# Performance work log

Measured on AMD Instinct MI355X. Metric: run time of the kernel, lower is better.

The kernel has to match this reference:

```python
import jax, jax.numpy as jnp
import numpy as np

N_NODES = 25000
N_EDGES = 320000
IN_FEAT = 64
OUT_FEAT = 64
NUM_HEADS = 5
NUM_RELS = 20
NUM_BASES = 10


def setup_inputs() -> dict:
    key = jax.random.key(0)
    ks = jax.random.split(key, 8)
    feat = jax.random.normal(ks[0], (N_NODES, IN_FEAT), dtype=jnp.float32)
    src = jax.random.randint(ks[1], (N_EDGES,), 0, N_NODES, dtype=jnp.int64 if jax.config.jax_enable_x64 else jnp.int32)
    dst = jax.random.randint(ks[2], (N_EDGES,), 0, N_NODES, dtype=src.dtype)
    edge_type = jax.random.randint(ks[3], (N_EDGES,), 0, NUM_RELS, dtype=src.dtype)
    fc_w = jax.random.normal(ks[4], (IN_FEAT, OUT_FEAT), dtype=jnp.float32) * (2.0 / np.sqrt(IN_FEAT + OUT_FEAT))
    self_fc_w = jax.random.normal(ks[5], (IN_FEAT, NUM_HEADS * OUT_FEAT), dtype=jnp.float32) * (2.0 / np.sqrt(IN_FEAT + NUM_HEADS * OUT_FEAT))
    attention_weight = jax.random.normal(ks[6], (NUM_BASES, 2 * OUT_FEAT, NUM_HEADS), dtype=jnp.float32) * (2.0 / np.sqrt(2 * OUT_FEAT + NUM_HEADS))
    w_comp = jax.random.normal(ks[7], (NUM_RELS, NUM_BASES), dtype=jnp.float32) * (2.0 / np.sqrt(NUM_RELS + NUM_BASES))
    return {"feat": feat, "src": src, "dst": dst, "edge_type": edge_type,
            "fc_w": fc_w, "self_fc_w": self_fc_w,
            "attention_weight": attention_weight, "w_comp": w_comp}


def reference(feat, src, dst, edge_type, fc_w, self_fc_w, attention_weight, w_comp):
    # node projections
    z = feat @ fc_w                      # [N, F]
    self_z = feat @ self_fc_w            # [N, H*F]
    # basis-composed per-relation attention matrices: [R, 2F, H]
    attn_fcs = jnp.einsum('rb,bfh->rfh', w_comp, attention_weight)
    # per-edge attention: cat(src_z, dst_z) bmm gathered relation matrix
    z2 = jnp.concatenate([z[src], z[dst]], axis=1)          # [E, 2F]
    w_e = attn_fcs[edge_type]                                # [E, 2F, H] irregular gather
    att = jax.nn.leaky_relu(jnp.einsum('ef,efh->eh', z2, w_e), negative_slope=0.01)  # [E, H]
    # message = outer(att, src_z) flattened, segment-summed over dst
    msg = (att[:, :, None] * z[src][:, None, :]).reshape(att.shape[0], -1)  # [E, H*F]
    h = jax.ops.segment_sum(msg, dst, num_segments=feat.shape[0])            # [N, H*F]
    h = h + self_z  # self interaction; activation is None
    return h
```

## Files before the change

### kernel.cpp

```cpp
#include <hip/hip_runtime.h>
#include <hip/hip_bf16.h>

#define N_NODES 25000
#define N_EDGES 320000
#define F 64
#define H 5
#define R 20
#define B 10
#define HF 320
#define MPAD 25008
#define CAP 64

typedef __attribute__((ext_vector_type(8))) short short8;
typedef __attribute__((ext_vector_type(4))) short short4v;
typedef __attribute__((ext_vector_type(4))) float float4v;

__device__ __forceinline__ float ldf(const void* p, int f32, int i) {
    if (f32) return ((const float*)p)[i];
    else     return __bfloat162float(((const __hip_bfloat16*)p)[i]);
}
__device__ __forceinline__ int ldi(const void* p, int i64, int i) {
    if (i64) return ((const int*)p)[2 * i];
    else     return ((const int*)p)[i];
}
__device__ __forceinline__ float b2f(unsigned short u) {
    union { unsigned u32; float f; } v; v.u32 = ((unsigned)u) << 16; return v.f;
}
__device__ __forceinline__ short f2bs(float x) {
    __hip_bfloat16 v = __float2bfloat16(x); return *(short*)&v;
}

__device__ __forceinline__ int probe_f32(const void* feat_raw) {
    unsigned w = ((const unsigned*)feat_raw)[threadIdx.x & 63];
    unsigned e = (w >> 7) & 0xFF;
    unsigned long long m = __ballot(e >= 110 && e <= 140);
    return __popcll(m) < 32;
}
__device__ __forceinline__ int probe_i64(const void* src_raw) {
    unsigned v = ((const unsigned*)src_raw)[2 * (threadIdx.x & 63) + 1];
    unsigned long long m = __ballot(v == 0);
    return __popcll(m) > 32;
}

__global__ void k0_setup(const void* __restrict__ feat,
                         const void* __restrict__ fcw, const void* __restrict__ sfw,
                         const void* __restrict__ aw, const void* __restrict__ wc,
                         __hip_bfloat16* __restrict__ Wpack,
                         __hip_bfloat16* __restrict__ W2pack,
                         int* __restrict__ cnt) {
    const int f32 = probe_f32(feat);
    const int b = blockIdx.x, tid = threadIdx.x;
    if (b < 176) {
        const int idx = b * 256 + tid;
        if (idx < 24576) {
            int j = idx & 7, lane = (idx >> 3) & 63, fq = idx >> 9;
            int q = fq & 1, t = fq >> 1;
            int k = (q ? 32 : 0) + ((lane >> 4) << 3) + j;
            int c = t * 16 + (lane & 15);
            float v = (c < HF) ? ldf(sfw, f32, k * HF + c) : ldf(fcw, f32, k * F + (c - HF));
            Wpack[idx] = __float2bfloat16(v);
        } else if (idx < 24576 + 20480) {
            int id2 = idx - 24576;
            int j = id2 & 7, lane = (id2 >> 3) & 63, fq = id2 >> 9;
            int q = fq & 1, t = fq >> 1;
            int k = (q ? 32 : 0) + ((lane >> 4) << 3) + j;
            int c = t * 16 + (lane & 15);
            int r = c >> 4, part = (c >> 3) & 1, h = c & 7;
            float acc = 0.f;
            if (h < H) {
#pragma unroll
                for (int bb = 0; bb < B; ++bb)
                    acc += ldf(wc, f32, r * B + bb) *
                           ldf(aw, f32, bb * (2 * F * H) + (part * F + k) * H + h);
            }
            W2pack[id2] = __float2bfloat16(acc);
        }
    } else {
        const int i = (b - 176) * 256 + tid;
        if (i < N_NODES) cnt[i] = 0;
    }
}

__global__ __launch_bounds__(256) void k2_gemm(const void* __restrict__ feat,
                                               const void* __restrict__ srcp,
                                               const void* __restrict__ dstp,
                                               const void* __restrict__ etp,
                                               const __hip_bfloat16* __restrict__ Wpack,
                                               const __hip_bfloat16* __restrict__ W2pack,
                                               __hip_bfloat16* __restrict__ selfz,
                                               __hip_bfloat16* __restrict__ zc,
                                               __hip_bfloat16* __restrict__ a_src,
                                               __hip_bfloat16* __restrict__ a_dst,
                                               int* __restrict__ cnt,
                                               unsigned* __restrict__ perm) {
    __shared__ short zl[16][66];
    const int tid = threadIdx.x;

    if (blockIdx.x >= 1563) {
        const int i64 = probe_i64(srcp);
        const int e = (blockIdx.x - 1563) * 256 + tid;
        if (e < N_EDGES) {
            int d = ldi(dstp, i64, e);
            int s = ldi(srcp, i64, e);
            int r = ldi(etp, i64, e);
            int pos = atomicAdd(&cnt[d], 1);
            if (pos < CAP) perm[d * CAP + pos] = ((unsigned)r << 16) | (unsigned)s;
        }
        return;
    }

    const int f32 = probe_f32(feat);
    const int wave = tid >> 6, lane = tid & 63;
    const int quad = lane >> 4, col = lane & 15;
    const int r0 = blockIdx.x * 16;
    int am = r0 + col;
    if (am >= N_NODES) am = N_NODES - 1;
    const int row = r0 + col;

    short8 a0, a1;
    if (f32) {
        const float* Af = (const float*)feat;
        float4v f0 = *(const float4v*)(Af + am * F + quad * 8);
        float4v f1 = *(const float4v*)(Af + am * F + quad * 8 + 4);
        float4v g0 = *(const float4v*)(Af + am * F + 32 + quad * 8);
        float4v g1 = *(const float4v*)(Af + am * F + 32 + quad * 8 + 4);
#pragma unroll
        for (int j = 0; j < 4; ++j) {
            a0[j] = f2bs(f0[j]); a0[j + 4] = f2bs(f1[j]);
            a1[j] = f2bs(g0[j]); a1[j + 4] = f2bs(g1[j]);
        }
    } else {
        const __hip_bfloat16* A = (const __hip_bfloat16*)feat;
        a0 = *(const short8*)(A + am * F + quad * 8);
        a1 = *(const short8*)(A + am * F + 32 + quad * 8);
    }

    const short8* Wp = (const short8*)Wpack;

    {
        const int t = 20 + wave;
        short8 b0 = Wp[(t * 2 + 0) * 64 + lane];
        short8 b1 = Wp[(t * 2 + 1) * 64 + lane];
        float4v acc = {0.f, 0.f, 0.f, 0.f};
        acc = __builtin_amdgcn_mfma_f32_16x16x32_bf16(b0, a0, acc, 0, 0, 0);
        acc = __builtin_amdgcn_mfma_f32_16x16x32_bf16(b1, a1, acc, 0, 0, 0);
        short4v pv;
#pragma unroll
        for (int j = 0; j < 4; ++j) pv[j] = f2bs(acc[j]);
        const int cb = wave * 16 + quad * 4;
        *(short4v*)(zc + row * F + cb) = pv;
        *(short4v*)&zl[col][cb] = pv;
    }
    __syncthreads();

    short8 c0 = *(const short8*)&zl[col][quad * 8];
    short8 c1 = *(const short8*)&zl[col][32 + quad * 8];

#pragma unroll
    for (int tt = 0; tt < 5; ++tt) {
        const int t = wave * 5 + tt;
        short8 b0 = Wp[(t * 2 + 0) * 64 + lane];
        short8 b1 = Wp[(t * 2 + 1) * 64 + lane];
        float4v acc = {0.f, 0.f, 0.f, 0.f};
        acc = __builtin_amdgcn_mfma_f32_16x16x32_bf16(b0, a0, acc, 0, 0, 0);
        acc = __builtin_amdgcn_mfma_f32_16x16x32_bf16(b1, a1, acc, 0, 0, 0);
        short4v pv;
#pragma unroll
        for (int j = 0; j < 4; ++j) pv[j] = f2bs(acc[j]);
        *(short4v*)(selfz + row * HF + t * 16 + quad * 4) = pv;
    }

    const short8* W2p = (const short8*)W2pack;
    __hip_bfloat16* dsta = (quad & 2) ? a_dst : a_src;
    const int hoff = (quad & 1) * 4;
#pragma unroll
    for (int tt = 0; tt < 5; ++tt) {
        const int t = wave * 5 + tt;
        short8 b0 = W2p[(t * 2 + 0) * 64 + lane];
        short8 b1 = W2p[(t * 2 + 1) * 64 + lane];
        float4v acc = {0.f, 0.f, 0.f, 0.f};
        acc = __builtin_amdgcn_mfma_f32_16x16x32_bf16(b0, c0, acc, 0, 0, 0);
        acc = __builtin_amdgcn_mfma_f32_16x16x32_bf16(b1, c1, acc, 0, 0, 0);
        short4v pv;
#pragma unroll
        for (int j = 0; j < 4; ++j) pv[j] = f2bs(acc[j]);
        *(short4v*)(dsta + row * 160 + t * 8 + hoff) = pv;
    }
}

__global__ __launch_bounds__(256) void k4_agg(const void* __restrict__ feat_raw,
                                              const __hip_bfloat16* __restrict__ selfz,
                                              const unsigned short* __restrict__ zc,
                                              const __hip_bfloat16* __restrict__ a_src,
                                              const __hip_bfloat16* __restrict__ a_dst,
                                              const int* __restrict__ cnt,
                                              const unsigned* __restrict__ perm,
                                              void* __restrict__ out) {
    __shared__ short sdv[4][160];
    const int f32 = probe_f32(feat_raw);
    const int tid = threadIdx.x;
    const int wid = tid >> 6, lane = tid & 63;
    const int d = blockIdx.x * 4 + wid;

    if (lane < 20)
        *(short8*)&sdv[wid][lane * 8] = *(const short8*)((const short*)a_dst + d * 160 + lane * 8);

    int mypk = (int)perm[d * CAP + lane];
    int n = cnt[d];
    if (n > CAP) n = CAP;
    __syncthreads();

    const short* as = (const short*)a_src;

    float acc[H] = {0.f, 0.f, 0.f, 0.f, 0.f};
    int e = 0;
    for (; e + 4 <= n; e += 4) {
        int s_[4], r_[4];
#pragma unroll
        for (int u = 0; u < 4; ++u) {
            unsigned pk = (unsigned)__shfl(mypk, e + u);
            s_[u] = (int)(pk & 0xFFFFu); r_[u] = (int)(pk >> 16);
        }
        short8 sv[4];
        float zs[4];
#pragma unroll
        for (int u = 0; u < 4; ++u) sv[u] = *(const short8*)(as + s_[u] * 160 + r_[u] * 8);
#pragma unroll
        for (int u = 0; u < 4; ++u) zs[u] = b2f(zc[s_[u] * F + lane]);
        short8 dv[4];
#pragma unroll
        for (int u = 0; u < 4; ++u) dv[u] = *(const short8*)&sdv[wid][r_[u] * 8];
#pragma unroll
        for (int u = 0; u < 4; ++u) {
#pragma unroll
            for (int h = 0; h < H; ++h) {
                float t = b2f((unsigned short)sv[u][h]) + b2f((unsigned short)dv[u][h]);
                acc[h] += fmaxf(t, 0.01f * t) * zs[u];
            }
        }
    }
    for (; e < n; ++e) {
        unsigned pk = (unsigned)__shfl(mypk, e);
        const int s = (int)(pk & 0xFFFFu), r = (int)(pk >> 16);
        short8 sv = *(const short8*)(as + s * 160 + r * 8);
        const float zs = b2f(zc[s * F + lane]);
        short8 dv = *(const short8*)&sdv[wid][r * 8];
#pragma unroll
        for (int h = 0; h < H; ++h) {
            float t = b2f((unsigned short)sv[h]) + b2f((unsigned short)dv[h]);
            acc[h] += fmaxf(t, 0.01f * t) * zs;
        }
    }

    const int ob = d * HF + lane;
    if (f32) {
        float* o = (float*)out;
#pragma unroll
        for (int h = 0; h < H; ++h)
            o[ob + h * F] = acc[h] + __bfloat162float(selfz[ob + h * F]);
    } else {
        __hip_bfloat16* o = (__hip_bfloat16*)out;
#pragma unroll
        for (int h = 0; h < H; ++h)
            o[ob + h * F] = __float2bfloat16(acc[h] + __bfloat162float(selfz[ob + h * F]));
    }
}

extern "C" void kernel_launch(void* const* d_in, const int* in_sizes, int n_in,
                              void* d_out, int out_size, void* d_ws, size_t ws_size,
                              hipStream_t stream) {
    const void* feat = d_in[0];
    const void* src  = d_in[1];
    const void* dst  = d_in[2];
    const void* et   = d_in[3];
    const void* fcw  = d_in[4];
    const void* sfw  = d_in[5];
    const void* aw   = d_in[6];
    const void* wc   = d_in[7];

    char* w = (char*)d_ws;
    __hip_bfloat16* selfz  = (__hip_bfloat16*)w;  w += (size_t)MPAD * HF * 2;
    __hip_bfloat16* zc     = (__hip_bfloat16*)w;  w += (size_t)MPAD * F * 2;
    __hip_bfloat16* a_src  = (__hip_bfloat16*)w;  w += (size_t)MPAD * 160 * 2;
    __hip_bfloat16* a_dst  = (__hip_bfloat16*)w;  w += (size_t)MPAD * 160 * 2;
    __hip_bfloat16* Wpack  = (__hip_bfloat16*)w;  w += 24576 * 2;
    __hip_bfloat16* W2pack = (__hip_bfloat16*)w;  w += 20480 * 2;
    unsigned* perm = (unsigned*)w;                w += (size_t)N_NODES * CAP * 4;
    int* cnt       = (int*)w;

    k0_setup<<<176 + (N_NODES + 255) / 256, 256, 0, stream>>>(feat, fcw, sfw, aw, wc,
                                                              Wpack, W2pack, cnt);
    k2_gemm<<<1563 + (N_EDGES + 255) / 256, 256, 0, stream>>>(feat, src, dst, et,
                                                              Wpack, W2pack, selfz, zc,
                                                              a_src, a_dst, cnt, perm);
    k4_agg<<<N_NODES / 4, 256, 0, stream>>>(feat, selfz, (const unsigned short*)zc,
                                            a_src, a_dst, cnt, perm, d_out);
}
```

Before: 140.6 us.

## Tile GEMM blocks over 64 rows and precompute per-edge attention in LDS

```diff
diff --git a/kernel.cpp b/kernel.cpp
--- a/kernel.cpp
+++ b/kernel.cpp
@@ -8,12 +8,14 @@
 #define R 20
 #define B 10
 #define HF 320
-#define MPAD 25008
+#define GEMMB 391
+#define MPAD 25024
 #define CAP 64
 
 typedef __attribute__((ext_vector_type(8))) short short8;
 typedef __attribute__((ext_vector_type(4))) short short4v;
 typedef __attribute__((ext_vector_type(4))) float float4v;
+typedef __attribute__((ext_vector_type(2))) float float2v;
 
 __device__ __forceinline__ float ldf(const void* p, int f32, int i) {
     if (f32) return ((const float*)p)[i];
@@ -93,12 +95,12 @@
                                                __hip_bfloat16* __restrict__ a_dst,
                                                int* __restrict__ cnt,
                                                unsigned* __restrict__ perm) {
-    __shared__ short zl[16][66];
+    __shared__ short zl[64][66];
     const int tid = threadIdx.x;
 
-    if (blockIdx.x >= 1563) {
+    if (blockIdx.x >= GEMMB) {
         const int i64 = probe_i64(srcp);
-        const int e = (blockIdx.x - 1563) * 256 + tid;
+        const int e = (blockIdx.x - GEMMB) * 256 + tid;
         if (e < N_EDGES) {
             int d = ldi(dstp, i64, e);
             int s = ldi(srcp, i64, e);
@@ -112,27 +114,29 @@
     const int f32 = probe_f32(feat);
     const int wave = tid >> 6, lane = tid & 63;
     const int quad = lane >> 4, col = lane & 15;
-    const int r0 = blockIdx.x * 16;
-    int am = r0 + col;
-    if (am >= N_NODES) am = N_NODES - 1;
-    const int row = r0 + col;
-
-    short8 a0, a1;
-    if (f32) {
-        const float* Af = (const float*)feat;
-        float4v f0 = *(const float4v*)(Af + am * F + quad * 8);
-        float4v f1 = *(const float4v*)(Af + am * F + quad * 8 + 4);
-        float4v g0 = *(const float4v*)(Af + am * F + 32 + quad * 8);
-        float4v g1 = *(const float4v*)(Af + am * F + 32 + quad * 8 + 4);
-#pragma unroll
-        for (int j = 0; j < 4; ++j) {
-            a0[j] = f2bs(f0[j]); a0[j + 4] = f2bs(f1[j]);
-            a1[j] = f2bs(g0[j]); a1[j + 4] = f2bs(g1[j]);
-        }
-    } else {
-        const __hip_bfloat16* A = (const __hip_bfloat16*)feat;
-        a0 = *(const short8*)(A + am * F + quad * 8);
-        a1 = *(const short8*)(A + am * F + 32 + quad * 8);
+    const int r0 = blockIdx.x * 64;
+
+    short8 a0g[4], a1g[4];
+#pragma unroll
+    for (int g = 0; g < 4; ++g) {
+        int am = r0 + g * 16 + col;
+        if (am >= N_NODES) am = N_NODES - 1;
+        if (f32) {
+            const float* Af = (const float*)feat;
+            float4v f0 = *(const float4v*)(Af + am * F + quad * 8);
+            float4v f1 = *(const float4v*)(Af + am * F + quad * 8 + 4);
+            float4v g0 = *(const float4v*)(Af + am * F + 32 + quad * 8);
+            float4v g1 = *(const float4v*)(Af + am * F + 32 + quad * 8 + 4);
+#pragma unroll
+            for (int j = 0; j < 4; ++j) {
+                a0g[g][j] = f2bs(f0[j]); a0g[g][j + 4] = f2bs(f1[j]);
+                a1g[g][j] = f2bs(g0[j]); a1g[g][j + 4] = f2bs(g1[j]);
+            }
+        } else {
+            const __hip_bfloat16* A = (const __hip_bfloat16*)feat;
+            a0g[g] = *(const short8*)(A + am * F + quad * 8);
+            a1g[g] = *(const short8*)(A + am * F + 32 + quad * 8);
+        }
     }
 
     const short8* Wp = (const short8*)Wpack;
@@ -141,33 +145,45 @@
         const int t = 20 + wave;
         short8 b0 = Wp[(t * 2 + 0) * 64 + lane];
         short8 b1 = Wp[(t * 2 + 1) * 64 + lane];
-        float4v acc = {0.f, 0.f, 0.f, 0.f};
-        acc = __builtin_amdgcn_mfma_f32_16x16x32_bf16(b0, a0, acc, 0, 0, 0);
-        acc = __builtin_amdgcn_mfma_f32_16x16x32_bf16(b1, a1, acc, 0, 0, 0);
-        short4v pv;
-#pragma unroll
-        for (int j = 0; j < 4; ++j) pv[j] = f2bs(acc[j]);
         const int cb = wave * 16 + quad * 4;
-        *(short4v*)(zc + row * F + cb) = pv;
-        *(short4v*)&zl[col][cb] = pv;
+#pragma unroll
+        for (int g = 0; g < 4; ++g) {
+            float4v acc = {0.f, 0.f, 0.f, 0.f};
+            acc = __builtin_amdgcn_mfma_f32_16x16x32_bf16(b0, a0g[g], acc, 0, 0, 0);
+            acc = __builtin_amdgcn_mfma_f32_16x16x32_bf16(b1, a1g[g], acc, 0, 0, 0);
+            short4v pv;
+#pragma unroll
+            for (int j = 0; j < 4; ++j) pv[j] = f2bs(acc[j]);
+            const int row = r0 + g * 16 + col;
+            *(short4v*)(zc + row * F + cb) = pv;
+            *(short4v*)&zl[g * 16 + col][cb] = pv;
+        }
     }
     __syncthreads();
 
-    short8 c0 = *(const short8*)&zl[col][quad * 8];
-    short8 c1 = *(const short8*)&zl[col][32 + quad * 8];
+    short8 c0g[4], c1g[4];
+#pragma unroll
+    for (int g = 0; g < 4; ++g) {
+        c0g[g] = *(const short8*)&zl[g * 16 + col][quad * 8];
+        c1g[g] = *(const short8*)&zl[g * 16 + col][32 + quad * 8];
+    }
 
 #pragma unroll
     for (int tt = 0; tt < 5; ++tt) {
         const int t = wave * 5 + tt;
         short8 b0 = Wp[(t * 2 + 0) * 64 + lane];
         short8 b1 = Wp[(t * 2 + 1) * 64 + lane];
-        float4v acc = {0.f, 0.f, 0.f, 0.f};
-        acc = __builtin_amdgcn_mfma_f32_16x16x32_bf16(b0, a0, acc, 0, 0, 0);
-        acc = __builtin_amdgcn_mfma_f32_16x16x32_bf16(b1, a1, acc, 0, 0, 0);
-        short4v pv;
-#pragma unroll
-        for (int j = 0; j < 4; ++j) pv[j] = f2bs(acc[j]);
-        *(short4v*)(selfz + row * HF + t * 16 + quad * 4) = pv;
+#pragma unroll
+        for (int g = 0; g < 4; ++g) {
+            float4v acc = {0.f, 0.f, 0.f, 0.f};
+            acc = __builtin_amdgcn_mfma_f32_16x16x32_bf16(b0, a0g[g], acc, 0, 0, 0);
+            acc = __builtin_amdgcn_mfma_f32_16x16x32_bf16(b1, a1g[g], acc, 0, 0, 0);
+            short4v pv;
+#pragma unroll
+            for (int j = 0; j < 4; ++j) pv[j] = f2bs(acc[j]);
+            const int row = r0 + g * 16 + col;
+            *(short4v*)(selfz + row * HF + t * 16 + quad * 4) = pv;
+        }
     }
 
     const short8* W2p = (const short8*)W2pack;
@@ -178,13 +194,17 @@
         const int t = wave * 5 + tt;
         short8 b0 = W2p[(t * 2 + 0) * 64 + lane];
         short8 b1 = W2p[(t * 2 + 1) * 64 + lane];
-        float4v acc = {0.f, 0.f, 0.f, 0.f};
-        acc = __builtin_amdgcn_mfma_f32_16x16x32_bf16(b0, c0, acc, 0, 0, 0);
-        acc = __builtin_amdgcn_mfma_f32_16x16x32_bf16(b1, c1, acc, 0, 0, 0);
-        short4v pv;
-#pragma unroll
-        for (int j = 0; j < 4; ++j) pv[j] = f2bs(acc[j]);
-        *(short4v*)(dsta + row * 160 + t * 8 + hoff) = pv;
+#pragma unroll
+        for (int g = 0; g < 4; ++g) {
+            float4v acc = {0.f, 0.f, 0.f, 0.f};
+            acc = __builtin_amdgcn_mfma_f32_16x16x32_bf16(b0, c0g[g], acc, 0, 0, 0);
+            acc = __builtin_amdgcn_mfma_f32_16x16x32_bf16(b1, c1g[g], acc, 0, 0, 0);
+            short4v pv;
+#pragma unroll
+            for (int j = 0; j < 4; ++j) pv[j] = f2bs(acc[j]);
+            const int row = r0 + g * 16 + col;
+            *(short4v*)(dsta + row * 160 + t * 8 + hoff) = pv;
+        }
     }
 }
 
@@ -197,6 +217,7 @@
                                               const unsigned* __restrict__ perm,
                                               void* __restrict__ out) {
     __shared__ short sdv[4][160];
+    __shared__ float satt[4][CAP][8];
     const int f32 = probe_f32(feat_raw);
     const int tid = threadIdx.x;
     const int wid = tid >> 6, lane = tid & 63;
@@ -204,52 +225,58 @@
 
     if (lane < 20)
         *(short8*)&sdv[wid][lane * 8] = *(const short8*)((const short*)a_dst + d * 160 + lane * 8);
-
-    int mypk = (int)perm[d * CAP + lane];
+    const unsigned pk = perm[d * CAP + lane];
+    const int s_l = (int)(pk & 0xFFFFu), r_l = (int)(pk >> 16);
     int n = cnt[d];
     if (n > CAP) n = CAP;
     __syncthreads();
 
     const short* as = (const short*)a_src;
 
+    if (lane < n) {
+        short8 sv = *(const short8*)(as + s_l * 160 + r_l * 8);
+        short8 dv = *(const short8*)&sdv[wid][r_l * 8];
+        float av[H];
+#pragma unroll
+        for (int h = 0; h < H; ++h) {
+            float t = b2f((unsigned short)sv[h]) + b2f((unsigned short)dv[h]);
+            av[h] = fmaxf(t, 0.01f * t);
+        }
+        float4v w0 = {av[0], av[1], av[2], av[3]};
+        *(float4v*)&satt[wid][lane][0] = w0;
+        float2v w1 = {av[4], __int_as_float(s_l)};
+        *(float2v*)&satt[wid][lane][4] = w1;
+    }
+    __syncthreads();
+
     float acc[H] = {0.f, 0.f, 0.f, 0.f, 0.f};
     int e = 0;
     for (; e + 4 <= n; e += 4) {
-        int s_[4], r_[4];
+        float4v A[4]; float2v Bv[4];
 #pragma unroll
         for (int u = 0; u < 4; ++u) {
-            unsigned pk = (unsigned)__shfl(mypk, e + u);
-            s_[u] = (int)(pk & 0xFFFFu); r_[u] = (int)(pk >> 16);
-        }
-        short8 sv[4];
+            A[u] = *(const float4v*)&satt[wid][e + u][0];
+            Bv[u] = *(const float2v*)&satt[wid][e + u][4];
+        }
         float zs[4];
 #pragma unroll
-        for (int u = 0; u < 4; ++u) sv[u] = *(const short8*)(as + s_[u] * 160 + r_[u] * 8);
-#pragma unroll
-        for (int u = 0; u < 4; ++u) zs[u] = b2f(zc[s_[u] * F + lane]);
-        short8 dv[4];
-#pragma unroll
-        for (int u = 0; u < 4; ++u) dv[u] = *(const short8*)&sdv[wid][r_[u] * 8];
+        for (int u = 0; u < 4; ++u)
+            zs[u] = b2f(zc[__float_as_int(Bv[u][1]) * F + lane]);
 #pragma unroll
         for (int u = 0; u < 4; ++u) {
-#pragma unroll
-            for (int h = 0; h < H; ++h) {
-                float t = b2f((unsigned short)sv[u][h]) + b2f((unsigned short)dv[u][h]);
-                acc[h] += fmaxf(t, 0.01f * t) * zs[u];
-            }
+            acc[0] += A[u][0] * zs[u];
+            acc[1] += A[u][1] * zs[u];
+            acc[2] += A[u][2] * zs[u];
+            acc[3] += A[u][3] * zs[u];
+            acc[4] += Bv[u][0] * zs[u];
         }
     }
     for (; e < n; ++e) {
-        unsigned pk = (unsigned)__shfl(mypk, e);
-        const int s = (int)(pk & 0xFFFFu), r = (int)(pk >> 16);
-        short8 sv = *(const short8*)(as + s * 160 + r * 8);
-        const float zs = b2f(zc[s * F + lane]);
-        short8 dv = *(const short8*)&sdv[wid][r * 8];
-#pragma unroll
-        for (int h = 0; h < H; ++h) {
-            float t = b2f((unsigned short)sv[h]) + b2f((unsigned short)dv[h]);
-            acc[h] += fmaxf(t, 0.01f * t) * zs;
-        }
+        float4v A = *(const float4v*)&satt[wid][e][0];
+        float2v Bv = *(const float2v*)&satt[wid][e][4];
+        float zs = b2f(zc[__float_as_int(Bv[1]) * F + lane]);
+        acc[0] += A[0] * zs; acc[1] += A[1] * zs; acc[2] += A[2] * zs;
+        acc[3] += A[3] * zs; acc[4] += Bv[0] * zs;
     }
 
     const int ob = d * HF + lane;
@@ -290,9 +317,9 @@
 
     k0_setup<<<176 + (N_NODES + 255) / 256, 256, 0, stream>>>(feat, fcw, sfw, aw, wc,
                                                               Wpack, W2pack, cnt);
-    k2_gemm<<<1563 + (N_EDGES + 255) / 256, 256, 0, stream>>>(feat, src, dst, et,
-                                                              Wpack, W2pack, selfz, zc,
-                                                              a_src, a_dst, cnt, perm);
+    k2_gemm<<<GEMMB + (N_EDGES + 255) / 256, 256, 0, stream>>>(feat, src, dst, et,
+                                                               Wpack, W2pack, selfz, zc,
+                                                               a_src, a_dst, cnt, perm);
     k4_agg<<<N_NODES / 4, 256, 0, stream>>>(feat, selfz, (const unsigned short*)zc,
                                             a_src, a_dst, cnt, perm, d_out);
 }
```

Measured after the change: 134.5 us (median of 2 runs). 4.3% less time.

## Fuse three kernels into one persistent kernel with grid barriers

Applied to the files above, without the earlier changes.

```diff
diff --git a/kernel.cpp b/kernel.cpp
--- a/kernel.cpp
+++ b/kernel.cpp
@@ -8,12 +8,16 @@
 #define R 20
 #define B 10
 #define HF 320
-#define MPAD 25008
+#define MPAD 25024
 #define CAP 64
+#define GRID 1024
+#define GEMMV 1563
+#define SCATV 1250
 
 typedef __attribute__((ext_vector_type(8))) short short8;
 typedef __attribute__((ext_vector_type(4))) short short4v;
 typedef __attribute__((ext_vector_type(4))) float float4v;
+typedef __attribute__((ext_vector_type(2))) float float2v;
 
 __device__ __forceinline__ float ldf(const void* p, int f32, int i) {
     if (f32) return ((const float*)p)[i];
@@ -42,227 +46,237 @@
     return __popcll(m) > 32;
 }
 
-__global__ void k0_setup(const void* __restrict__ feat,
-                         const void* __restrict__ fcw, const void* __restrict__ sfw,
-                         const void* __restrict__ aw, const void* __restrict__ wc,
-                         __hip_bfloat16* __restrict__ Wpack,
-                         __hip_bfloat16* __restrict__ W2pack,
-                         int* __restrict__ cnt) {
+__device__ __forceinline__ void gridbar(int* bar) {
+    __syncthreads();
+    if (threadIdx.x == 0) {
+        __threadfence();
+        atomicAdd(bar, 1);
+        while (__hip_atomic_load(bar, __ATOMIC_RELAXED, __HIP_MEMORY_SCOPE_AGENT) < GRID)
+            __builtin_amdgcn_s_sleep(2);
+        __threadfence();
+    }
+    __syncthreads();
+}
+
+__global__ __launch_bounds__(256, 4) void mega(
+    const void* __restrict__ feat, const void* __restrict__ srcp,
+    const void* __restrict__ dstp, const void* __restrict__ etp,
+    const void* __restrict__ fcw, const void* __restrict__ sfw,
+    const void* __restrict__ aw, const void* __restrict__ wc,
+    __hip_bfloat16* __restrict__ Wpack, __hip_bfloat16* __restrict__ W2pack,
+    __hip_bfloat16* __restrict__ selfz, __hip_bfloat16* __restrict__ zc,
+    __hip_bfloat16* __restrict__ a_src, __hip_bfloat16* __restrict__ a_dst,
+    int* __restrict__ cnt, unsigned* __restrict__ perm,
+    int* __restrict__ bar, void* __restrict__ out)
+{
+    __shared__ union SM {
+        short zl[16][66];
+        struct P2 { short sdv[4][160]; float satt[4][CAP][8]; } p2;
+    } sm;
+
+    const int tid = threadIdx.x;
     const int f32 = probe_f32(feat);
-    const int b = blockIdx.x, tid = threadIdx.x;
-    if (b < 176) {
-        const int idx = b * 256 + tid;
-        if (idx < 24576) {
-            int j = idx & 7, lane = (idx >> 3) & 63, fq = idx >> 9;
-            int q = fq & 1, t = fq >> 1;
-            int k = (q ? 32 : 0) + ((lane >> 4) << 3) + j;
-            int c = t * 16 + (lane & 15);
-            float v = (c < HF) ? ldf(sfw, f32, k * HF + c) : ldf(fcw, f32, k * F + (c - HF));
-            Wpack[idx] = __float2bfloat16(v);
-        } else if (idx < 24576 + 20480) {
-            int id2 = idx - 24576;
-            int j = id2 & 7, lane = (id2 >> 3) & 63, fq = id2 >> 9;
-            int q = fq & 1, t = fq >> 1;
-            int k = (q ? 32 : 0) + ((lane >> 4) << 3) + j;
-            int c = t * 16 + (lane & 15);
-            int r = c >> 4, part = (c >> 3) & 1, h = c & 7;
-            float acc = 0.f;
-            if (h < H) {
-#pragma unroll
-                for (int bb = 0; bb < B; ++bb)
-                    acc += ldf(wc, f32, r * B + bb) *
-                           ldf(aw, f32, bb * (2 * F * H) + (part * F + k) * H + h);
-            }
-            W2pack[id2] = __float2bfloat16(acc);
-        }
-    } else {
-        const int i = (b - 176) * 256 + tid;
-        if (i < N_NODES) cnt[i] = 0;
-    }
-}
-
-__global__ __launch_bounds__(256) void k2_gemm(const void* __restrict__ feat,
-                                               const void* __restrict__ srcp,
-                                               const void* __restrict__ dstp,
-                                               const void* __restrict__ etp,
-                                               const __hip_bfloat16* __restrict__ Wpack,
-                                               const __hip_bfloat16* __restrict__ W2pack,
-                                               __hip_bfloat16* __restrict__ selfz,
-                                               __hip_bfloat16* __restrict__ zc,
-                                               __hip_bfloat16* __restrict__ a_src,
-                                               __hip_bfloat16* __restrict__ a_dst,
-                                               int* __restrict__ cnt,
-                                               unsigned* __restrict__ perm) {
-    __shared__ short zl[16][66];
-    const int tid = threadIdx.x;
-
-    if (blockIdx.x >= 1563) {
-        const int i64 = probe_i64(srcp);
-        const int e = (blockIdx.x - 1563) * 256 + tid;
-        if (e < N_EDGES) {
-            int d = ldi(dstp, i64, e);
-            int s = ldi(srcp, i64, e);
-            int r = ldi(etp, i64, e);
-            int pos = atomicAdd(&cnt[d], 1);
-            if (pos < CAP) perm[d * CAP + pos] = ((unsigned)r << 16) | (unsigned)s;
-        }
-        return;
-    }
-
-    const int f32 = probe_f32(feat);
+    const int i64 = probe_i64(srcp);
     const int wave = tid >> 6, lane = tid & 63;
     const int quad = lane >> 4, col = lane & 15;
-    const int r0 = blockIdx.x * 16;
-    int am = r0 + col;
-    if (am >= N_NODES) am = N_NODES - 1;
-    const int row = r0 + col;
-
-    short8 a0, a1;
-    if (f32) {
-        const float* Af = (const float*)feat;
-        float4v f0 = *(const float4v*)(Af + am * F + quad * 8);
-        float4v f1 = *(const float4v*)(Af + am * F + quad * 8 + 4);
-        float4v g0 = *(const float4v*)(Af + am * F + 32 + quad * 8);
-        float4v g1 = *(const float4v*)(Af + am * F + 32 + quad * 8 + 4);
-#pragma unroll
-        for (int j = 0; j < 4; ++j) {
-            a0[j] = f2bs(f0[j]); a0[j + 4] = f2bs(f1[j]);
-            a1[j] = f2bs(g0[j]); a1[j + 4] = f2bs(g1[j]);
-        }
-    } else {
-        const __hip_bfloat16* A = (const __hip_bfloat16*)feat;
-        a0 = *(const short8*)(A + am * F + quad * 8);
-        a1 = *(const short8*)(A + am * F + 32 + quad * 8);
+
+    {
+        const int vb = blockIdx.x;
+        if (vb < 176) {
+            const int idx = vb * 256 + tid;
+            if (idx < 24576) {
+                int j = idx & 7, ln = (idx >> 3) & 63, fq = idx >> 9;
+                int q = fq & 1, t = fq >> 1;
+                int k = (q ? 32 : 0) + ((ln >> 4) << 3) + j;
+                int c = t * 16 + (ln & 15);
+                float v = (c < HF) ? ldf(sfw, f32, k * HF + c) : ldf(fcw, f32, k * F + (c - HF));
+                Wpack[idx] = __float2bfloat16(v);
+            } else if (idx < 24576 + 20480) {
+                int id2 = idx - 24576;
+                int j = id2 & 7, ln = (id2 >> 3) & 63, fq = id2 >> 9;
+                int q = fq & 1, t = fq >> 1;
+                int k = (q ? 32 : 0) + ((ln >> 4) << 3) + j;
+                int c = t * 16 + (ln & 15);
+                int r = c >> 4, part = (c >> 3) & 1, h = c & 7;
+                float acc = 0.f;
+                if (h < H) {
+#pragma unroll
+                    for (int bb = 0; bb < B; ++bb)
+                        acc += ldf(wc, f32, r * B + bb) *
+                               ldf(aw, f32, bb * (2 * F * H) + (part * F + k) * H + h);
+                }
+                W2pack[id2] = __float2bfloat16(acc);
+            }
+        } else if (vb < 274) {
+            const int i = (vb - 176) * 256 + tid;
+            if (i < N_NODES) cnt[i] = 0;
+        }
     }
-
-    const short8* Wp = (const short8*)Wpack;
-
-    {
-        const int t = 20 + wave;
-        short8 b0 = Wp[(t * 2 + 0) * 64 + lane];
-        short8 b1 = Wp[(t * 2 + 1) * 64 + lane];
-        float4v acc = {0.f, 0.f, 0.f, 0.f};
-        acc = __builtin_amdgcn_mfma_f32_16x16x32_bf16(b0, a0, acc, 0, 0, 0);
-        acc = __builtin_amdgcn_mfma_f32_16x16x32_bf16(b1, a1, acc, 0, 0, 0);
-        short4v pv;
-#pragma unroll
-        for (int j = 0; j < 4; ++j) pv[j] = f2bs(acc[j]);
-        const int cb = wave * 16 + quad * 4;
-        *(short4v*)(zc + row * F + cb) = pv;
-        *(short4v*)&zl[col][cb] = pv;
+    gridbar(&bar[0]);
+
+    for (int vb = blockIdx.x; vb < GEMMV + SCATV; vb += GRID) {
+        if (vb >= GEMMV) {
+            const int e = (vb - GEMMV) * 256 + tid;
+            if (e < N_EDGES) {
+                int d = ldi(dstp, i64, e);
+                int s = ldi(srcp, i64, e);
+                int r = ldi(etp, i64, e);
+                int pos = atomicAdd(&cnt[d], 1);
+                if (pos < CAP) perm[d * CAP + pos] = ((unsigned)r << 16) | (unsigned)s;
+            }
+            continue;
+        }
+
+        int am = vb * 16 + col;
+        if (am >= N_NODES) am = N_NODES - 1;
+        const int row = vb * 16 + col;
+
+        short8 a0, a1;
+        if (f32) {
+            const float* Af = (const float*)feat;
+            float4v f0 = *(const float4v*)(Af + am * F + quad * 8);
+            float4v f1 = *(const float4v*)(Af + am * F + quad * 8 + 4);
+            float4v g0 = *(const float4v*)(Af + am * F + 32 + quad * 8);
+            float4v g1 = *(const float4v*)(Af + am * F + 32 + quad * 8 + 4);
+#pragma unroll
+            for (int j = 0; j < 4; ++j) {
+                a0[j] = f2bs(f0[j]); a0[j + 4] = f2bs(f1[j]);
+                a1[j] = f2bs(g0[j]); a1[j + 4] = f2bs(g1[j]);
+            }
+        } else {
+            const __hip_bfloat16* A = (const __hip_bfloat16*)feat;
+            a0 = *(const short8*)(A + am * F + quad * 8);
+            a1 = *(const short8*)(A + am * F + 32 + quad * 8);
+        }
+
+        const short8* Wp = (const short8*)Wpack;
+
+        {
+            const int t = 20 + wave;
+            short8 b0 = Wp[(t * 2 + 0) * 64 + lane];
+            short8 b1 = Wp[(t * 2 + 1) * 64 + lane];
+            float4v acc = {0.f, 0.f, 0.f, 0.f};
+            acc = __builtin_amdgcn_mfma_f32_16x16x32_bf16(b0, a0, acc, 0, 0, 0);
+            acc = __builtin_amdgcn_mfma_f32_16x16x32_bf16(b1, a1, acc, 0, 0, 0);
+            short4v pv;
+#pragma unroll
+            for (int j = 0; j < 4; ++j) pv[j] = f2bs(acc[j]);
+            const int cb = wave * 16 + quad * 4;
+            *(short4v*)(zc + row * F + cb) = pv;
+            *(short4v*)&sm.zl[col][cb] = pv;
+        }
+        __syncthreads();
+
+        short8 c0 = *(const short8*)&sm.zl[col][quad * 8];
+        short8 c1 = *(const short8*)&sm.zl[col][32 + quad * 8];
+
+#pragma unroll
+        for (int tt = 0; tt < 5; ++tt) {
+            const int t = wave * 5 + tt;
+            short8 b0 = Wp[(t * 2 + 0) * 64 + lane];
+            short8 b1 = Wp[(t * 2 + 1) * 64 + lane];
+            float4v acc = {0.f, 0.f, 0.f, 0.f};
+            acc = __builtin_amdgcn_mfma_f32_16x16x32_bf16(b0, a0, acc, 0, 0, 0);
+            acc = __builtin_amdgcn_mfma_f32_16x16x32_bf16(b1, a1, acc, 0, 0, 0);
+            short4v pv;
+#pragma unroll
+            for (int j = 0; j < 4; ++j) pv[j] = f2bs(acc[j]);
+            *(short4v*)(selfz + row * HF + t * 16 + quad * 4) = pv;
+        }
+
+        const short8* W2p = (const short8*)W2pack;
+        __hip_bfloat16* dsta = (quad & 2) ? a_dst : a_src;
+        const int hoff = (quad & 1) * 4;
+#pragma unroll
+        for (int tt = 0; tt < 5; ++tt) {
+            const int t = wave * 5 + tt;
+            short8 b0 = W2p[(t * 2 + 0) * 64 + lane];
+            short8 b1 = W2p[(t * 2 + 1) * 64 + lane];
+            float4v acc = {0.f, 0.f, 0.f, 0.f};
+            acc = __builtin_amdgcn_mfma_f32_16x16x32_bf16(b0, c0, acc, 0, 0, 0);
+            acc = __builtin_amdgcn_mfma_f32_16x16x32_bf16(b1, c1, acc, 0, 0, 0);
+            short4v pv;
+#pragma unroll
+            for (int j = 0; j < 4; ++j) pv[j] = f2bs(acc[j]);
+            *(short4v*)(dsta + row * 160 + t * 8 + hoff) = pv;
+        }
+        __syncthreads();
     }
-    __syncthreads();
-
-    short8 c0 = *(const short8*)&zl[col][quad * 8];
-    short8 c1 = *(const short8*)&zl[col][32 + quad * 8];
-
-#pragma unroll
-    for (int tt = 0; tt < 5; ++tt) {
-        const int t = wave * 5 + tt;
-        short8 b0 = Wp[(t * 2 + 0) * 64 + lane];
-        short8 b1 = Wp[(t * 2 + 1) * 64 + lane];
-        float4v acc = {0.f, 0.f, 0.f, 0.f};
-        acc = __builtin_amdgcn_mfma_f32_16x16x32_bf16(b0, a0, acc, 0, 0, 0);
-        acc = __builtin_amdgcn_mfma_f32_16x16x32_bf16(b1, a1, acc, 0, 0, 0);
-        short4v pv;
-#pragma unroll
-        for (int j = 0; j < 4; ++j) pv[j] = f2bs(acc[j]);
-        *(short4v*)(selfz + row * HF + t * 16 + quad * 4) = pv;
-    }
-
-    const short8* W2p = (const short8*)W2pack;
-    __hip_bfloat16* dsta = (quad & 2) ? a_dst : a_src;
-    const int hoff = (quad & 1) * 4;
-#pragma unroll
-    for (int tt = 0; tt < 5; ++tt) {
-        const int t = wave * 5 + tt;
-        short8 b0 = W2p[(t * 2 + 0) * 64 + lane];
-        short8 b1 = W2p[(t * 2 + 1) * 64 + lane];
-        float4v acc = {0.f, 0.f, 0.f, 0.f};
-        acc = __builtin_amdgcn_mfma_f32_16x16x32_bf16(b0, c0, acc, 0, 0, 0);
-        acc = __builtin_amdgcn_mfma_f32_16x16x32_bf16(b1, c1, acc, 0, 0, 0);
-        short4v pv;
-#pragma unroll
-        for (int j = 0; j < 4; ++j) pv[j] = f2bs(acc[j]);
-        *(short4v*)(dsta + row * 160 + t * 8 + hoff) = pv;
-    }
-}
-
-__global__ __launch_bounds__(256) void k4_agg(const void* __restrict__ feat_raw,
-                                              const __hip_bfloat16* __restrict__ selfz,
-                                              const unsigned short* __restrict__ zc,
-                                              const __hip_bfloat16* __restrict__ a_src,
-                                              const __hip_bfloat16* __restrict__ a_dst,
-                                              const int* __restrict__ cnt,
-                                              const unsigned* __restrict__ perm,
-                                              void* __restrict__ out) {
-    __shared__ short sdv[4][160];
-    const int f32 = probe_f32(feat_raw);
-    const int tid = threadIdx.x;
-    const int wid = tid >> 6, lane = tid & 63;
-    const int d = blockIdx.x * 4 + wid;
-
-    if (lane < 20)
-        *(short8*)&sdv[wid][lane * 8] = *(const short8*)((const short*)a_dst + d * 160 + lane * 8);
-
-    int mypk = (int)perm[d * CAP + lane];
-    int n = cnt[d];
-    if (n > CAP) n = CAP;
-    __syncthreads();
-
-    const short* as = (const short*)a_src;
-
-    float acc[H] = {0.f, 0.f, 0.f, 0.f, 0.f};
-    int e = 0;
-    for (; e + 4 <= n; e += 4) {
-        int s_[4], r_[4];
-#pragma unroll
-        for (int u = 0; u < 4; ++u) {
-            unsigned pk = (unsigned)__shfl(mypk, e + u);
-            s_[u] = (int)(pk & 0xFFFFu); r_[u] = (int)(pk >> 16);
-        }
-        short8 sv[4];
-        float zs[4];
-#pragma unroll
-        for (int u = 0; u < 4; ++u) sv[u] = *(const short8*)(as + s_[u] * 160 + r_[u] * 8);
-#pragma unroll
-        for (int u = 0; u < 4; ++u) zs[u] = b2f(zc[s_[u] * F + lane]);
-        short8 dv[4];
-#pragma unroll
-        for (int u = 0; u < 4; ++u) dv[u] = *(const short8*)&sdv[wid][r_[u] * 8];
-#pragma unroll
-        for (int u = 0; u < 4; ++u) {
+    gridbar(&bar[1]);
+
+    for (int vb = blockIdx.x; vb < N_NODES / 4; vb += GRID) {
+        const int d = vb * 4 + wave;
+
+        if (lane < 20)
+            *(short8*)&sm.p2.sdv[wave][lane * 8] =
+                *(const short8*)((const short*)a_dst + d * 160 + lane * 8);
+        const unsigned pk = perm[d * CAP + lane];
+        const int s_l = (int)(pk & 0xFFFFu), r_l = (int)(pk >> 16);
+        int n = cnt[d];
+        if (n > CAP) n = CAP;
+        __syncthreads();
+
+        const short* as = (const short*)a_src;
+
+        if (lane < n) {
+            short8 sv = *(const short8*)(as + s_l * 160 + r_l * 8);
+            short8 dv = *(const short8*)&sm.p2.sdv[wave][r_l * 8];
+            float av[H];
 #pragma unroll
             for (int h = 0; h < H; ++h) {
-                float t = b2f((unsigned short)sv[u][h]) + b2f((unsigned short)dv[u][h]);
-                acc[h] += fmaxf(t, 0.01f * t) * zs[u];
-            }
-        }
-    }
-    for (; e < n; ++e) {
-        unsigned pk = (unsigned)__shfl(mypk, e);
-        const int s = (int)(pk & 0xFFFFu), r = (int)(pk >> 16);
-        short8 sv = *(const short8*)(as + s * 160 + r * 8);
-        const float zs = b2f(zc[s * F + lane]);
-        short8 dv = *(const short8*)&sdv[wid][r * 8];
-#pragma unroll
-        for (int h = 0; h < H; ++h) {
-            float t = b2f((unsigned short)sv[h]) + b2f((unsigned short)dv[h]);
-            acc[h] += fmaxf(t, 0.01f * t) * zs;
-        }
-    }
-
-    const int ob = d * HF + lane;
-    if (f32) {
-        float* o = (float*)out;
-#pragma unroll
-        for (int h = 0; h < H; ++h)
-            o[ob + h * F] = acc[h] + __bfloat162float(selfz[ob + h * F]);
-    } else {
-        __hip_bfloat16* o = (__hip_bfloat16*)out;
-#pragma unroll
-        for (int h = 0; h < H; ++h)
-            o[ob + h * F] = __float2bfloat16(acc[h] + __bfloat162float(selfz[ob + h * F]));
+                float t = b2f((unsigned short)sv[h]) + b2f((unsigned short)dv[h]);
+                av[h] = fmaxf(t, 0.01f * t);
+            }
+            float4v w0 = {av[0], av[1], av[2], av[3]};
+            *(float4v*)&sm.p2.satt[wave][lane][0] = w0;
+            float2v w1 = {av[4], __int_as_float(s_l)};
+            *(float2v*)&sm.p2.satt[wave][lane][4] = w1;
+        }
+        __syncthreads();
+
+        float acc[H] = {0.f, 0.f, 0.f, 0.f, 0.f};
+        int e = 0;
+        for (; e + 4 <= n; e += 4) {
+            float4v A[4]; float2v Bv[4];
+#pragma unroll
+            for (int u = 0; u < 4; ++u) {
+                A[u] = *(const float4v*)&sm.p2.satt[wave][e + u][0];
+                Bv[u] = *(const float2v*)&sm.p2.satt[wave][e + u][4];
+            }
+            float zs[4];
+#pragma unroll
+            for (int u = 0; u < 4; ++u)
+                zs[u] = b2f(((const unsigned short*)zc)[__float_as_int(Bv[u][1]) * F + lane]);
+#pragma unroll
+            for (int u = 0; u < 4; ++u) {
+                acc[0] += A[u][0] * zs[u];
+                acc[1] += A[u][1] * zs[u];
+                acc[2] += A[u][2] * zs[u];
+                acc[3] += A[u][3] * zs[u];
+                acc[4] += Bv[u][0] * zs[u];
+            }
+        }
+        for (; e < n; ++e) {
+            float4v A = *(const float4v*)&sm.p2.satt[wave][e][0];
+            float2v Bv = *(const float2v*)&sm.p2.satt[wave][e][4];
+            float zs = b2f(((const unsigned short*)zc)[__float_as_int(Bv[1]) * F + lane]);
+            acc[0] += A[0] * zs; acc[1] += A[1] * zs; acc[2] += A[2] * zs;
+            acc[3] += A[3] * zs; acc[4] += Bv[0] * zs;
+        }
+
+        const int ob = d * HF + lane;
+        if (f32) {
+            float* o = (float*)out;
+#pragma unroll
+            for (int h = 0; h < H; ++h)
+                o[ob + h * F] = acc[h] + __bfloat162float(selfz[ob + h * F]);
+        } else {
+            __hip_bfloat16* o = (__hip_bfloat16*)out;
+#pragma unroll
+            for (int h = 0; h < H; ++h)
+                o[ob + h * F] = __float2bfloat16(acc[h] + __bfloat162float(selfz[ob + h * F]));
+        }
+        __syncthreads();
     }
 }
 
@@ -286,13 +300,11 @@
     __hip_bfloat16* Wpack  = (__hip_bfloat16*)w;  w += 24576 * 2;
     __hip_bfloat16* W2pack = (__hip_bfloat16*)w;  w += 20480 * 2;
     unsigned* perm = (unsigned*)w;                w += (size_t)N_NODES * CAP * 4;
-    int* cnt       = (int*)w;
-
-    k0_setup<<<176 + (N_NODES + 255) / 256, 256, 0, stream>>>(feat, fcw, sfw, aw, wc,
-                                                              Wpack, W2pack, cnt);
-    k2_gemm<<<1563 + (N_EDGES + 255) / 256, 256, 0, stream>>>(feat, src, dst, et,
-                                                              Wpack, W2pack, selfz, zc,
-                                                              a_src, a_dst, cnt, perm);
-    k4_agg<<<N_NODES / 4, 256, 0, stream>>>(feat, selfz, (const unsigned short*)zc,
-                                            a_src, a_dst, cnt, perm, d_out);
-}
+    int* cnt       = (int*)w;                     w += (size_t)((N_NODES + 8) / 8) * 8 * 4;
+    int* bar       = (int*)w;
+
+    hipMemsetAsync(bar, 0, 16, stream);
+    mega<<<GRID, 256, 0, stream>>>(feat, src, dst, et, fcw, sfw, aw, wc,
+                                   Wpack, W2pack, selfz, zc, a_src, a_dst,
+                                   cnt, perm, bar, d_out);
+}
```

Result: slower. 365.5 us (+159.9%).
